# Performance work log

Measured on AMD Instinct MI355X. Metric: run time of the kernel, lower is better.

The kernel has to match this reference:

```python
import jax, jax.numpy as jnp
from jax import lax
import numpy as np

B, T, D = 8192, 187, 1
H, C = 128, 5


def setup_inputs() -> dict:
    key = jax.random.key(0)
    k1, k2, k3, k4 = jax.random.split(key, 4)
    x = jax.random.normal(k1, (B, T, D), dtype=jnp.float32)
    # SimpleRNN params: kernel W [D,H], recurrent kernel U [H,H] (orthogonal-ish), bias b [H]
    W = jax.random.normal(k2, (D, H), dtype=jnp.float32) * (1.0 / np.sqrt(D))
    U = jax.random.normal(k3, (H, H), dtype=jnp.float32) * (1.0 / np.sqrt(H))
    b = jnp.zeros((H,), dtype=jnp.float32)
    # Dense head params
    Wd = jax.random.normal(k4, (H, C), dtype=jnp.float32) * (1.0 / np.sqrt(H))
    bd = jnp.zeros((C,), dtype=jnp.float32)
    return {"x": x, "W": W, "U": U, "b": b, "Wd": Wd, "bd": bd}


def reference(x, W, U, b, Wd, bd):
    # SimpleRNN (tanh) recurrence over time, returning final hidden state only
    # (return_sequences=False, dropout inactive at inference).
    h0 = jnp.zeros((x.shape[0], U.shape[0]), dtype=x.dtype)
    xt_seq = jnp.swapaxes(x, 0, 1)  # [T, B, D]

    def step(h, xt):
        h_new = jnp.tanh(xt @ W + h @ U + b)
        return h_new, None

    hT, _ = lax.scan(step, h0, xt_seq)
    # Dense softmax classifier head
    logits = hT @ Wd + bd  # [B, C]
    return jax.nn.softmax(logits, axis=-1)
```

## Files before the change

kernel.cpp:

```cpp
#include <hip/hip_runtime.h>
#include <hip/hip_bf16.h>


#define BT 8192
#define TS 187
#define HD 128
#define NC 5

typedef float    f32x4  __attribute__((ext_vector_type(4)));
typedef _Float16 f16x8  __attribute__((ext_vector_type(8)));
typedef __fp16   fp16x2 __attribute__((ext_vector_type(2)));
typedef unsigned int u32;
typedef u32      u32x2  __attribute__((ext_vector_type(2)));

__device__ __forceinline__ float tanh_fast(float v) {
    float e = __expf(2.0f * v);
    float r = __builtin_amdgcn_rcpf(e + 1.0f);
    return fmaf(-2.0f, r, 1.0f);
}

__device__ __forceinline__ u32 pk16(float a, float b) {
    fp16x2 p = __builtin_amdgcn_cvt_pkrtz(a, b);
    return __builtin_bit_cast(u32, p);
}

union frag_u { f16x8 v; u32 w[4]; };

__device__ __forceinline__ void pin_frag(f16x8& f) {
    frag_u pu; pu.v = f;
    asm volatile("" : "+v"(pu.w[0]), "+v"(pu.w[1]), "+v"(pu.w[2]), "+v"(pu.w[3]));
    f = pu.v;
}

__global__ __launch_bounds__(512, 4)
void rnn_fused(const float* __restrict__ xg, const float* __restrict__ wg,
               const float* __restrict__ ug, const float* __restrict__ bg,
               const float* __restrict__ wdg, const float* __restrict__ bdg,
               float* __restrict__ outg)
{
    __shared__ u32   xb[2][4][64][4];
    __shared__ float lg[8][16][NC];

    const int tid  = threadIdx.x;
    const int w    = tid >> 6;
    const int lane = tid & 63;
    const int l15  = lane & 15;
    const int l4   = lane >> 4;
    const int b0   = blockIdx.x * 16;
    const int Tw   = w >> 1;
    const int hw   = w & 1;

    f16x8 uf0, uf1, uf2, uf3;
    {
        const int j = 16*w + l15;
        #pragma unroll
        for (int e = 0; e < 8; ++e) {
            const int i = 16*(e>>2) + 4*l4 + (e&3);
            uf0[e] = (_Float16)ug[(i      )*HD + j];
            uf1[e] = (_Float16)ug[(i + 32 )*HD + j];
            uf2[e] = (_Float16)ug[(i + 64 )*HD + j];
            uf3[e] = (_Float16)ug[(i + 96 )*HD + j];
        }
    }
    pin_frag(uf0); pin_frag(uf1); pin_frag(uf2); pin_frag(uf3);

    float wv[4], bv[4];
    #pragma unroll
    for (int q = 0; q < 4; ++q) {
        const int j = 16*w + 4*l4 + q;
        wv[q] = wg[j];
        bv[q] = bg[j];
    }

    f16x8 h0 = (f16x8)(_Float16)0.0f;
    f16x8 h1 = h0, h2 = h0, h3 = h0;

    const float* xrow = xg + (long)(b0 + l15) * TS;
    float xv = xrow[0];

    f32x4 acc;

    for (int s = 0; s < TS; ++s) {
        const int sn = (s + 1 < TS) ? s + 1 : TS - 1;
        float xnext = xrow[sn];

        #pragma unroll
        for (int q = 0; q < 4; ++q) acc[q] = fmaf(xv, wv[q], bv[q]);
        acc = __builtin_amdgcn_mfma_f32_16x16x32_f16(uf0, h0, acc, 0, 0, 0);
        acc = __builtin_amdgcn_mfma_f32_16x16x32_f16(uf1, h1, acc, 0, 0, 0);
        acc = __builtin_amdgcn_mfma_f32_16x16x32_f16(uf2, h2, acc, 0, 0, 0);
        acc = __builtin_amdgcn_mfma_f32_16x16x32_f16(uf3, h3, acc, 0, 0, 0);

        #pragma unroll
        for (int q = 0; q < 4; ++q) acc[q] = tanh_fast(acc[q]);

        u32x2 pk;
        pk[0] = pk16(acc[0], acc[1]);
        pk[1] = pk16(acc[2], acc[3]);
        *(u32x2*)&xb[s & 1][Tw][lane][2*hw] = pk;
        __syncthreads();

        h0 = *(const f16x8*)&xb[s & 1][0][lane][0];
        h1 = *(const f16x8*)&xb[s & 1][1][lane][0];
        h2 = *(const f16x8*)&xb[s & 1][2][lane][0];
        h3 = *(const f16x8*)&xb[s & 1][3][lane][0];

        xv = xnext;
    }

    float p[NC];
    #pragma unroll
    for (int c = 0; c < NC; ++c) p[c] = 0.0f;
    #pragma unroll
    for (int q = 0; q < 4; ++q) {
        const int j = 16*w + 4*l4 + q;
        #pragma unroll
        for (int c = 0; c < NC; ++c)
            p[c] = fmaf(acc[q], wdg[j*NC + c], p[c]);
    }
    #pragma unroll
    for (int c = 0; c < NC; ++c) {
        p[c] += __shfl_xor(p[c], 16, 64);
        p[c] += __shfl_xor(p[c], 32, 64);
    }
    if (l4 == 0) {
        #pragma unroll
        for (int c = 0; c < NC; ++c) lg[w][l15][c] = p[c];
    }
    __syncthreads();

    if (tid < 16) {
        float l[NC];
        #pragma unroll
        for (int c = 0; c < NC; ++c) {
            l[c] = bdg[c];
            #pragma unroll
            for (int ww = 0; ww < 8; ++ww) l[c] += lg[ww][tid][c];
        }
        float m = l[0];
        #pragma unroll
        for (int c = 1; c < NC; ++c) m = fmaxf(m, l[c]);
        float e[NC], ssum = 0.0f;
        #pragma unroll
        for (int c = 0; c < NC; ++c) { e[c] = __expf(l[c] - m); ssum += e[c]; }
        const float rs = 1.0f / ssum;
        #pragma unroll
        for (int c = 0; c < NC; ++c)
            outg[(long)(b0 + tid)*NC + c] = e[c] * rs;
    }
}

extern "C" void kernel_launch(void* const* d_in, const int* in_sizes, int n_in,
                              void* d_out, int out_size, void* d_ws, size_t ws_size,
                              hipStream_t stream) {
    const float* x  = (const float*)d_in[0];
    const float* W  = (const float*)d_in[1];
    const float* U  = (const float*)d_in[2];
    const float* b  = (const float*)d_in[3];
    const float* Wd = (const float*)d_in[4];
    const float* bd = (const float*)d_in[5];
    float* out = (float*)d_out;

    rnn_fused<<<BT / 16, 512, 0, stream>>>(x, W, U, b, Wd, bd, out);
}
```

Before: 86.63 us.

## Stage x in LDS, split MFMA chain into two accumulators, unroll by two

Each block preloads its 16x187 slice of x into shared memory with coalesced loads, so the loop no longer issues a scattered global load every timestep. The four dependent MFMAs are split into two independent accumulator chains that are summed before tanh, which shortens the serial latency on the recurrent critical path. The loop is manually unrolled by two so the double-buffer index is a constant. This costs about 12 KB of extra LDS per block, which may reduce occupancy, plus one extra add per element.

```diff
diff --git a/kernel.cpp b/kernel.cpp
--- a/kernel.cpp
+++ b/kernel.cpp
@@ -39,6 +39,7 @@
                float* __restrict__ outg)
 {
     __shared__ u32   xb[2][4][64][4];
+    __shared__ float xs[TS][16];
     __shared__ float lg[8][16][NC];
 
     const int tid  = threadIdx.x;
@@ -49,6 +50,15 @@
     const int b0   = blockIdx.x * 16;
     const int Tw   = w >> 1;
     const int hw   = w & 1;
+
+    #pragma unroll
+    for (int r = 0; r < 6; ++r) {
+        const int idx = r * 512 + tid;
+        const int bb  = idx / 192;
+        const int ss  = idx % 192;
+        if (ss < TS)
+            xs[ss][bb] = xg[(long)(b0 + bb) * TS + ss];
+    }
 
     f16x8 uf0, uf1, uf2, uf3;
     {
@@ -75,38 +85,42 @@
     f16x8 h0 = (f16x8)(_Float16)0.0f;
     f16x8 h1 = h0, h2 = h0, h3 = h0;
 
-    const float* xrow = xg + (long)(b0 + l15) * TS;
-    float xv = xrow[0];
+    __syncthreads();
+    float xv = xs[0][l15];
 
     f32x4 acc;
 
-    for (int s = 0; s < TS; ++s) {
-        const int sn = (s + 1 < TS) ? s + 1 : TS - 1;
-        float xnext = xrow[sn];
+#define STEP(BUF, SN)                                                       \
+    {                                                                       \
+        const float xnext = xs[(SN)][l15];                                  \
+        f32x4 a0, a1;                                                       \
+        _Pragma("unroll") for (int q = 0; q < 4; ++q) {                     \
+            a0[q] = fmaf(xv, wv[q], bv[q]); a1[q] = 0.0f;                   \
+        }                                                                   \
+        a0 = __builtin_amdgcn_mfma_f32_16x16x32_f16(uf0, h0, a0, 0, 0, 0);  \
+        a1 = __builtin_amdgcn_mfma_f32_16x16x32_f16(uf2, h2, a1, 0, 0, 0);  \
+        a0 = __builtin_amdgcn_mfma_f32_16x16x32_f16(uf1, h1, a0, 0, 0, 0);  \
+        a1 = __builtin_amdgcn_mfma_f32_16x16x32_f16(uf3, h3, a1, 0, 0, 0);  \
+        _Pragma("unroll") for (int q = 0; q < 4; ++q)                       \
+            acc[q] = tanh_fast(a0[q] + a1[q]);                              \
+        u32x2 pk;                                                           \
+        pk[0] = pk16(acc[0], acc[1]);                                       \
+        pk[1] = pk16(acc[2], acc[3]);                                       \
+        *(u32x2*)&xb[(BUF)][Tw][lane][2*hw] = pk;                           \
+        __syncthreads();                                                    \
+        h0 = *(const f16x8*)&xb[(BUF)][0][lane][0];                         \
+        h1 = *(const f16x8*)&xb[(BUF)][1][lane][0];                         \
+        h2 = *(const f16x8*)&xb[(BUF)][2][lane][0];                         \
+        h3 = *(const f16x8*)&xb[(BUF)][3][lane][0];                         \
+        xv = xnext;                                                         \
+    }
 
-        #pragma unroll
-        for (int q = 0; q < 4; ++q) acc[q] = fmaf(xv, wv[q], bv[q]);
-        acc = __builtin_amdgcn_mfma_f32_16x16x32_f16(uf0, h0, acc, 0, 0, 0);
-        acc = __builtin_amdgcn_mfma_f32_16x16x32_f16(uf1, h1, acc, 0, 0, 0);
-        acc = __builtin_amdgcn_mfma_f32_16x16x32_f16(uf2, h2, acc, 0, 0, 0);
-        acc = __builtin_amdgcn_mfma_f32_16x16x32_f16(uf3, h3, acc, 0, 0, 0);
-
-        #pragma unroll
-        for (int q = 0; q < 4; ++q) acc[q] = tanh_fast(acc[q]);
-
-        u32x2 pk;
-        pk[0] = pk16(acc[0], acc[1]);
-        pk[1] = pk16(acc[2], acc[3]);
-        *(u32x2*)&xb[s & 1][Tw][lane][2*hw] = pk;
-        __syncthreads();
-
-        h0 = *(const f16x8*)&xb[s & 1][0][lane][0];
-        h1 = *(const f16x8*)&xb[s & 1][1][lane][0];
-        h2 = *(const f16x8*)&xb[s & 1][2][lane][0];
-        h3 = *(const f16x8*)&xb[s & 1][3][lane][0];
-
-        xv = xnext;
+    for (int k = 0; k < 93; ++k) {
+        STEP(0, 2*k + 1);
+        STEP(1, 2*k + 2);
     }
+    STEP(0, TS - 1);
+#undef STEP
 
     float p[NC];
     #pragma unroll
```

After: 85.42 us. No clear change (-1.4%).
